# Kernel optimization log

Measured on AMD Instinct MI355X. Metric: run time of the kernel, lower is better.

Reference implementation:

```python
import jax, jax.numpy as jnp
import numpy as np

DIM = 512
NUM_HEADS = 8
B, NW, W = 8, 64, 64  # batch, num_windows, window_size


def setup_inputs() -> dict:
    key = jax.random.key(0)
    k1, k2, k3 = jax.random.split(key, 3)
    x = jax.random.normal(k1, (B, NW, W, DIM), dtype=jnp.float32)
    w_qkv = jax.random.normal(k2, (DIM, 3 * DIM), dtype=jnp.float32) * (DIM ** -0.5)
    w_proj = jax.random.normal(k3, (DIM, DIM), dtype=jnp.float32) * (DIM ** -0.5)
    b_proj = jnp.zeros((DIM,), dtype=jnp.float32)
    return {"x": x, "w_qkv": w_qkv, "w_proj": w_proj, "b_proj": b_proj}


def reference(x, w_qkv, w_proj, b_proj):
    batch, nw, w, dim = x.shape
    heads = NUM_HEADS
    dh = dim // heads
    scale = dh ** -0.5
    # qkv projection (no bias): [B, nW, W, 3*dim]
    qkv = jnp.einsum('bnwc,cd->bnwd', x, w_qkv)
    # -> [B, nW, W, 3, H, dh] -> [3, B, H, nW, W, dh]
    qkv = qkv.reshape(batch, nw, w, 3, heads, dh)
    qkv = jnp.transpose(qkv, (3, 0, 4, 1, 2, 5))
    q, k, v = qkv[0], qkv[1], qkv[2]
    # attention logits per window: [B, H, nW, W, W]
    attn = jnp.einsum('bhnqd,bhnkd->bhnqk', q, k) * scale
    attn = jax.nn.softmax(attn, axis=-1)
    # [B, H, nW, W, dh]
    out = jnp.einsum('bhnqk,bhnkd->bhnqd', attn, v)
    # faithful raw reshape (no transpose), matching the TF source
    out = out.reshape(batch, nw, w, dim)
    return jnp.einsum('bnwc,cd->bnwd', out, w_proj) + b_proj
```

## Files before the change

kernel.cpp:

```cpp
#include <hip/hip_runtime.h>
#include <hip/hip_bf16.h>

typedef __bf16 bf16_t;
typedef __bf16 bf16x4 __attribute__((ext_vector_type(4)));
typedef __bf16 bf16x8 __attribute__((ext_vector_type(8)));
typedef float f32x4 __attribute__((ext_vector_type(4)));
typedef float f32x16 __attribute__((ext_vector_type(16)));

#define GLOAD_LDS16(gp, lp) __builtin_amdgcn_global_load_lds( \
    (const __attribute__((address_space(1))) void*)(gp),      \
    (__attribute__((address_space(3))) void*)(lp), 16, 0, 0)

#define VMCNT(n) asm volatile("s_waitcnt vmcnt(" #n ")" ::: "memory")
#define SCHED_FENCE() __builtin_amdgcn_sched_barrier(0)
#define BARRIER() __builtin_amdgcn_s_barrier()

__device__ __forceinline__ int swz64(int row, int col) {
    return row * 64 + (col ^ ((row & 7) << 3));
}

__global__ __launch_bounds__(256) void transpose_cast_kernel(
    const float* __restrict__ src, bf16_t* __restrict__ dst, int R, int C)
{
    __shared__ float tile[32][33];
    const int bx = blockIdx.x;
    const int by = blockIdx.y;
    const int t  = threadIdx.x;
    const int i0 = t >> 5;
    const int j  = t & 31;
#pragma unroll
    for (int p = 0; p < 4; ++p) {
        int i = i0 + p * 8;
        tile[i][j] = src[(long)(by * 32 + i) * C + bx * 32 + j];
    }
    __syncthreads();
#pragma unroll
    for (int p = 0; p < 4; ++p) {
        int i = i0 + p * 8;
        dst[(long)(bx * 32 + i) * R + by * 32 + j] = (bf16_t)tile[j][i];
    }
}

__global__ __launch_bounds__(256) void cast_x_kernel(
    const float* __restrict__ src, bf16_t* __restrict__ dst, long n8)
{
    long i = (long)blockIdx.x * blockDim.x + threadIdx.x;
    const long stride = (long)gridDim.x * blockDim.x;
    for (; i < n8; i += stride) {
        const float* p = src + i * 8;
        f32x4 f0 = *(const f32x4*)p;
        f32x4 f1 = *(const f32x4*)(p + 4);
        bf16x8 o;
        o[0] = (bf16_t)f0[0]; o[1] = (bf16_t)f0[1];
        o[2] = (bf16_t)f0[2]; o[3] = (bf16_t)f0[3];
        o[4] = (bf16_t)f1[0]; o[5] = (bf16_t)f1[1];
        o[6] = (bf16_t)f1[2]; o[7] = (bf16_t)f1[3];
        *(bf16x8*)(dst + i * 8) = o;
    }
}

__global__ __launch_bounds__(256, 2) void qkv_attn_kernel(
    const bf16_t* __restrict__ xb,
    const bf16_t* __restrict__ wT,
    bf16_t* __restrict__ ao)
{
    __shared__ bf16_t arena[40960];
    bf16_t* const buf0 = arena;
    bf16_t* const buf1 = arena + 20480;

    const int id   = blockIdx.x;
    const int xcd  = id & 7;
    const int s    = id >> 3;
    const int pr   = xcd * 32 + (s >> 3);
    const int h    = s & 7;
    const int wid0 = pr * 2;

    const bf16_t* xw = xb + (long)wid0 * 64 * 512;

    const int t    = threadIdx.x;
    const int wv   = t >> 6;
    const int lane = t & 63;
    const int wm   = wv >> 1;
    const int wn   = wv & 1;
    const int l31  = lane & 31;
    const int l5   = lane >> 5;
    const int rlo  = lane >> 3;
    const int ch   = (lane & 7) ^ rlo;

    bf16_t* const lQw = arena +     0 + wm * 12288;
    bf16_t* const lKw = arena +  4096 + wm * 12288;
    bf16_t* const lVw = arena +  8192 + wm * 12288;
    bf16_t* const lPw = arena + 24576 + wm * 4096;

    auto stage = [&](bf16_t* buf, int k0) {
#pragma unroll
        for (int p = 0; p < 4; ++p) {
            const int rb = wv * 4 + p;
            GLOAD_LDS16(xw + (long)(rb * 8 + rlo) * 512 + k0 + ch * 8,
                        buf + rb * 512);
        }
#pragma unroll
        for (int j = 0; j < 6; ++j) {
            const int rb = wv * 6 + j;
            const int nr = rb * 8 + rlo;
            const int grow = ((nr >> 6) << 9) + h * 64 + (nr & 63);
            GLOAD_LDS16(wT + (long)grow * 512 + k0 + ch * 8,
                        buf + 8192 + rb * 512);
        }
    };

    f32x16 acc[2][3];
#pragma unroll
    for (int mi = 0; mi < 2; ++mi)
#pragma unroll
        for (int ni = 0; ni < 3; ++ni) acc[mi][ni] = (f32x16)0.0f;

    auto compute = [&](const bf16_t* lX, const bf16_t* lW) {
        __builtin_amdgcn_s_setprio(1);
#pragma unroll
        for (int ks = 0; ks < 64; ks += 16) {
            bf16x8 a0 = *(const bf16x8*)&lX[swz64(wm * 64 +  0 + l31, ks + l5 * 8)];
            bf16x8 a1 = *(const bf16x8*)&lX[swz64(wm * 64 + 32 + l31, ks + l5 * 8)];
#pragma unroll
            for (int ni = 0; ni < 3; ++ni) {
                bf16x8 b = *(const bf16x8*)&lW[swz64(wn * 96 + ni * 32 + l31, ks + l5 * 8)];
                acc[0][ni] = __builtin_amdgcn_mfma_f32_32x32x16_bf16(a0, b, acc[0][ni], 0, 0, 0);
                acc[1][ni] = __builtin_amdgcn_mfma_f32_32x32x16_bf16(a1, b, acc[1][ni], 0, 0, 0);
            }
        }
        __builtin_amdgcn_s_setprio(0);
    };

    stage(buf0, 0);
#pragma unroll 1
    for (int kc2 = 0; kc2 < 4; ++kc2) {
        const int kc = kc2 * 2;
        stage(buf1, (kc + 1) * 64);
        VMCNT(10);
        SCHED_FENCE();
        BARRIER();
        compute(buf0, buf0 + 8192);
        SCHED_FENCE();
        BARRIER();
        if (kc2 < 3) {
            stage(buf0, (kc + 2) * 64);
            VMCNT(10);
        } else {
            VMCNT(0);
        }
        SCHED_FENCE();
        BARRIER();
        compute(buf1, buf1 + 8192);
        SCHED_FENCE();
        BARRIER();
    }

#pragma unroll
    for (int mi = 0; mi < 2; ++mi) {
#pragma unroll
        for (int ni = 0; ni < 3; ++ni) {
            const int n = wn * 96 + ni * 32 + l31;
            const int g = n >> 6;
            const int c = n & 63;
            if (g == 2) {
#pragma unroll
                for (int rq = 0; rq < 4; ++rq) {
                    const int tk0 = mi * 32 + 8 * rq + 4 * l5;
                    bf16x4 pk;
                    pk[0] = (bf16_t)acc[mi][ni][rq * 4 + 0];
                    pk[1] = (bf16_t)acc[mi][ni][rq * 4 + 1];
                    pk[2] = (bf16_t)acc[mi][ni][rq * 4 + 2];
                    pk[3] = (bf16_t)acc[mi][ni][rq * 4 + 3];
                    *(bf16x4*)&lVw[swz64(c, tk0)] = pk;
                }
            } else {
#pragma unroll
                for (int r = 0; r < 16; ++r) {
                    const int tk = mi * 32 + (r & 3) + ((r >> 2) << 3) + (l5 << 2);
                    const bf16_t val = (bf16_t)acc[mi][ni][r];
                    if (g == 0) lQw[swz64(tk, c)] = val;
                    else        lKw[swz64(tk, c)] = val;
                }
            }
        }
    }
    __syncthreads();

    const int lr = lane & 15;
    const int q  = lane >> 4;
    const int qh = wn * 32;
    const float scale = 0.125f;

    f32x4 sA[2][4];
#pragma unroll
    for (int i = 0; i < 2; ++i)
#pragma unroll
        for (int j = 0; j < 4; ++j) sA[i][j] = (f32x4)0.0f;
#pragma unroll
    for (int ks = 0; ks < 64; ks += 32) {
        bf16x8 aq0 = *(const bf16x8*)&lQw[swz64(qh +  0 + lr, ks + q * 8)];
        bf16x8 aq1 = *(const bf16x8*)&lQw[swz64(qh + 16 + lr, ks + q * 8)];
#pragma unroll
        for (int j = 0; j < 4; ++j) {
            bf16x8 bk = *(const bf16x8*)&lKw[swz64(j * 16 + lr, ks + q * 8)];
            sA[0][j] = __builtin_amdgcn_mfma_f32_16x16x32_bf16(aq0, bk, sA[0][j], 0, 0, 0);
            sA[1][j] = __builtin_amdgcn_mfma_f32_16x16x32_bf16(aq1, bk, sA[1][j], 0, 0, 0);
        }
    }

#pragma unroll
    for (int i = 0; i < 2; ++i)
#pragma unroll
    for (int reg = 0; reg < 4; ++reg) {
        float m = fmaxf(fmaxf(sA[i][0][reg], sA[i][1][reg]),
                        fmaxf(sA[i][2][reg], sA[i][3][reg]));
#pragma unroll
        for (int d = 1; d < 16; d <<= 1) m = fmaxf(m, __shfl_xor(m, d));
        float p[4];
        float sum = 0.0f;
#pragma unroll
        for (int j = 0; j < 4; ++j) {
            p[j] = __expf((sA[i][j][reg] - m) * scale);
            sum += p[j];
        }
#pragma unroll
        for (int d = 1; d < 16; d <<= 1) sum += __shfl_xor(sum, d);
        const float inv = 1.0f / sum;
        const int row = qh + i * 16 + q * 4 + reg;
#pragma unroll
        for (int j = 0; j < 4; ++j)
            lPw[swz64(row, j * 16 + lr)] = (bf16_t)(p[j] * inv);
    }

    f32x4 o[2][4];
#pragma unroll
    for (int i = 0; i < 2; ++i)
#pragma unroll
        for (int d4 = 0; d4 < 4; ++d4) o[i][d4] = (f32x4)0.0f;
#pragma unroll
    for (int ks = 0; ks < 64; ks += 32) {
        bf16x8 ap0 = *(const bf16x8*)&lPw[swz64(qh +  0 + lr, ks + q * 8)];
        bf16x8 ap1 = *(const bf16x8*)&lPw[swz64(qh + 16 + lr, ks + q * 8)];
#pragma unroll
        for (int d4 = 0; d4 < 4; ++d4) {
            bf16x8 bv = *(const bf16x8*)&lVw[swz64(d4 * 16 + lr, ks + q * 8)];
            o[0][d4] = __builtin_amdgcn_mfma_f32_16x16x32_bf16(ap0, bv, o[0][d4], 0, 0, 0);
            o[1][d4] = __builtin_amdgcn_mfma_f32_16x16x32_bf16(ap1, bv, o[1][d4], 0, 0, 0);
        }
    }

    const int wid = wid0 + wm;
    const int bb  = wid >> 6;
    const int nw  = wid & 63;
    bf16_t* aop = ao + ((long)bb * 4096 + (long)h * 512 + nw * 8) * 512;
#pragma unroll
    for (int i = 0; i < 2; ++i)
#pragma unroll
    for (int d4 = 0; d4 < 4; ++d4)
#pragma unroll
    for (int reg = 0; reg < 4; ++reg) {
        const int wr = qh + i * 16 + q * 4 + reg;
        aop[(long)(wr >> 3) * 512 + (wr & 7) * 64 + d4 * 16 + lr] =
            (bf16_t)o[i][d4][reg];
    }
}

__global__ __launch_bounds__(256) void gemm2_kernel(
    const bf16_t* __restrict__ A,
    const bf16_t* __restrict__ Bt,
    const float*  __restrict__ bias,
    float* __restrict__ C,
    int M, int N, int K)
{
    __shared__ bf16_t arena[32768];
    bf16_t* const lA0 = arena;
    bf16_t* const lB0 = arena + 8192;
    bf16_t* const lA1 = arena + 16384;
    bf16_t* const lB1 = arena + 24576;

    const int tid  = threadIdx.x;
    const int wave = tid >> 6;
    const int lane = tid & 63;
    const int wm   = wave >> 1;
    const int wn   = wave & 1;
    const int lr   = lane & 15;
    const int q    = lane >> 4;
    const int rlo  = lane >> 3;
    const int ch   = (lane & 7) ^ rlo;

    const int id  = blockIdx.x;
    const int xcd = id & 7;
    const int s   = id >> 3;
    const int bm  = xcd * 32 + (s >> 2);
    const int bn  = s & 3;

    const long arow0 = (long)bm * 128;
    const long brow0 = (long)bn * 128;

    f32x4 acc[4][4];
#pragma unroll
    for (int i = 0; i < 4; ++i)
#pragma unroll
        for (int j = 0; j < 4; ++j) acc[i][j] = (f32x4)0.0f;

    auto stage = [&](bf16_t* bA, bf16_t* bB, long k0) {
#pragma unroll
        for (int p = 0; p < 4; ++p) {
            const int rb = wave * 4 + p;
            const int r  = rb * 8 + rlo;
            GLOAD_LDS16(A  + (arow0 + r) * (long)K + k0 + ch * 8, bA + rb * 512);
            GLOAD_LDS16(Bt + (brow0 + r) * (long)K + k0 + ch * 8, bB + rb * 512);
        }
    };

    auto compute = [&](const bf16_t* lA, const bf16_t* lB) {
        __builtin_amdgcn_s_setprio(1);
#pragma unroll
        for (int ks = 0; ks < 64; ks += 32) {
            bf16x8 af[4], bf[4];
#pragma unroll
            for (int i = 0; i < 4; ++i)
                af[i] = *(const bf16x8*)&lA[swz64(wm * 64 + i * 16 + lr, ks + q * 8)];
#pragma unroll
            for (int j = 0; j < 4; ++j)
                bf[j] = *(const bf16x8*)&lB[swz64(wn * 64 + j * 16 + lr, ks + q * 8)];
#pragma unroll
            for (int i = 0; i < 4; ++i)
#pragma unroll
                for (int j = 0; j < 4; ++j)
                    acc[i][j] = __builtin_amdgcn_mfma_f32_16x16x32_bf16(
                        af[i], bf[j], acc[i][j], 0, 0, 0);
        }
        __builtin_amdgcn_s_setprio(0);
    };

    stage(lA0, lB0, 0);
#pragma unroll 1
    for (int kt2 = 0; kt2 < 4; ++kt2) {
        const int kt = kt2 * 2;
        stage(lA1, lB1, (long)(kt + 1) * 64);
        VMCNT(8);
        SCHED_FENCE();
        BARRIER();
        compute(lA0, lB0);
        SCHED_FENCE();
        BARRIER();
        if (kt2 < 3) {
            stage(lA0, lB0, (long)(kt + 2) * 64);
            VMCNT(8);
        } else {
            VMCNT(0);
        }
        SCHED_FENCE();
        BARRIER();
        compute(lA1, lB1);
        SCHED_FENCE();
        BARRIER();
    }

#pragma unroll
    for (int i = 0; i < 4; ++i) {
        const long r = arow0 + wm * 64 + i * 16 + q * 4;
#pragma unroll
        for (int j = 0; j < 4; ++j) {
            const long c = brow0 + wn * 64 + j * 16 + lr;
            const float bv2 = bias[c];
#pragma unroll
            for (int reg = 0; reg < 4; ++reg) {
                C[(r + reg) * N + c] = acc[i][j][reg] + bv2;
            }
        }
    }
}

extern "C" void kernel_launch(void* const* d_in, const int* in_sizes, int n_in,
                              void* d_out, int out_size, void* d_ws, size_t ws_size,
                              hipStream_t stream)
{
    (void)in_sizes; (void)n_in; (void)out_size;
    const float* x     = (const float*)d_in[0];
    const float* wqkv  = (const float*)d_in[1];
    const float* wproj = (const float*)d_in[2];
    const float* bproj = (const float*)d_in[3];
    float* out = (float*)d_out;

    bf16_t* wT = (bf16_t*)d_ws;
    bf16_t* pT = wT + (size_t)1536 * 512;
    bf16_t* ao = pT + (size_t)512 * 512;

    const size_t base_elems = (size_t)1536 * 512 + (size_t)512 * 512
                            + (size_t)32768 * 512;
    const size_t xb_elems   = (size_t)32768 * 512;
    bf16_t* xb = (ws_size >= (base_elems + xb_elems) * sizeof(bf16_t))
               ? (ao + xb_elems)
               : (bf16_t*)d_out;

    transpose_cast_kernel<<<dim3(48, 16), 256, 0, stream>>>(wqkv, wT, 512, 1536);
    transpose_cast_kernel<<<dim3(16, 16), 256, 0, stream>>>(wproj, pT, 512, 512);
    cast_x_kernel<<<2048, 256, 0, stream>>>(x, xb, (long)32768 * 512 / 8);

    qkv_attn_kernel<<<2048, 256, 0, stream>>>(xb, wT, ao);

    gemm2_kernel<<<1024, 256, 0, stream>>>(
        ao, pT, bproj, out, 32768, 512, 512);
}
```

Before: 209.8 us.

## Load QKV GEMM X operand to registers and triple-buffer weights in LDS

In the fused QKV+attention kernel, the X tile is now loaded straight from global memory into double-buffered registers instead of being staged through LDS. Only the weight tiles go through LDS, now in a three-deep ring that needs one barrier per K-chunk instead of two. LDS use drops from 80KB to 72KB, with the P buffer aliased onto the Q region. In exchange, register pressure rises and the two wn-waves issue duplicate global loads for the same X rows.

```diff
diff --git a/kernel.cpp b/kernel.cpp
--- a/kernel.cpp
+++ b/kernel.cpp
@@ -64,9 +64,11 @@
     const bf16_t* __restrict__ wT,
     bf16_t* __restrict__ ao)
 {
-    __shared__ bf16_t arena[40960];
-    bf16_t* const buf0 = arena;
-    bf16_t* const buf1 = arena + 20480;
+    __shared__ bf16_t arena[36864];
+    bf16_t* const wb0 = arena;
+    bf16_t* const wb1 = arena + 12288;
+    bf16_t* const wb2 = arena + 24576;
+    bf16_t* const wb[3] = { wb0, wb1, wb2 };
 
     const int id   = blockIdx.x;
     const int xcd  = id & 7;
@@ -87,27 +89,29 @@
     const int rlo  = lane >> 3;
     const int ch   = (lane & 7) ^ rlo;
 
-    bf16_t* const lQw = arena +     0 + wm * 12288;
-    bf16_t* const lKw = arena +  4096 + wm * 12288;
-    bf16_t* const lVw = arena +  8192 + wm * 12288;
-    bf16_t* const lPw = arena + 24576 + wm * 4096;
-
-    auto stage = [&](bf16_t* buf, int k0) {
-#pragma unroll
-        for (int p = 0; p < 4; ++p) {
-            const int rb = wv * 4 + p;
-            GLOAD_LDS16(xw + (long)(rb * 8 + rlo) * 512 + k0 + ch * 8,
-                        buf + rb * 512);
-        }
+    bf16_t* const lQw = arena +    0 + wm * 12288;
+    bf16_t* const lKw = arena + 4096 + wm * 12288;
+    bf16_t* const lVw = arena + 8192 + wm * 12288;
+    bf16_t* const lPw = lQw;
+
+    auto stageW = [&](bf16_t* buf, int k0) {
 #pragma unroll
         for (int j = 0; j < 6; ++j) {
             const int rb = wv * 6 + j;
             const int nr = rb * 8 + rlo;
             const int grow = ((nr >> 6) << 9) + h * 64 + (nr & 63);
-            GLOAD_LDS16(wT + (long)grow * 512 + k0 + ch * 8,
-                        buf + 8192 + rb * 512);
+            GLOAD_LDS16(wT + (long)grow * 512 + k0 + ch * 8, buf + rb * 512);
         }
     };
+    auto loadx = [&](bf16x8* xr, int k0) {
+#pragma unroll
+        for (int ksi = 0; ksi < 4; ++ksi)
+#pragma unroll
+            for (int mi = 0; mi < 2; ++mi)
+                xr[ksi * 2 + mi] = *(const bf16x8*)(
+                    xw + (long)(wm * 64 + mi * 32 + l31) * 512
+                       + k0 + ksi * 16 + l5 * 8);
+    };
 
     f32x16 acc[2][3];
 #pragma unroll
@@ -115,45 +119,43 @@
 #pragma unroll
         for (int ni = 0; ni < 3; ++ni) acc[mi][ni] = (f32x16)0.0f;
 
-    auto compute = [&](const bf16_t* lX, const bf16_t* lW) {
+    auto compute = [&](const bf16x8* xr, const bf16_t* lW) {
         __builtin_amdgcn_s_setprio(1);
 #pragma unroll
-        for (int ks = 0; ks < 64; ks += 16) {
-            bf16x8 a0 = *(const bf16x8*)&lX[swz64(wm * 64 +  0 + l31, ks + l5 * 8)];
-            bf16x8 a1 = *(const bf16x8*)&lX[swz64(wm * 64 + 32 + l31, ks + l5 * 8)];
+        for (int ksi = 0; ksi < 4; ++ksi) {
+            const int ks = ksi * 16;
 #pragma unroll
             for (int ni = 0; ni < 3; ++ni) {
-                bf16x8 b = *(const bf16x8*)&lW[swz64(wn * 96 + ni * 32 + l31, ks + l5 * 8)];
-                acc[0][ni] = __builtin_amdgcn_mfma_f32_32x32x16_bf16(a0, b, acc[0][ni], 0, 0, 0);
-                acc[1][ni] = __builtin_amdgcn_mfma_f32_32x32x16_bf16(a1, b, acc[1][ni], 0, 0, 0);
+                bf16x8 b = *(const bf16x8*)&lW[swz64(wn * 96 + ni * 32 + l31,
+                                                    ks + l5 * 8)];
+                acc[0][ni] = __builtin_amdgcn_mfma_f32_32x32x16_bf16(
+                    xr[ksi * 2 + 0], b, acc[0][ni], 0, 0, 0);
+                acc[1][ni] = __builtin_amdgcn_mfma_f32_32x32x16_bf16(
+                    xr[ksi * 2 + 1], b, acc[1][ni], 0, 0, 0);
             }
         }
         __builtin_amdgcn_s_setprio(0);
     };
 
-    stage(buf0, 0);
-#pragma unroll 1
-    for (int kc2 = 0; kc2 < 4; ++kc2) {
-        const int kc = kc2 * 2;
-        stage(buf1, (kc + 1) * 64);
-        VMCNT(10);
+    bf16x8 xA[8], xB[8];
+    loadx(xA, 0);
+    stageW(wb0, 0);
+    stageW(wb1, 64);
+#pragma unroll
+    for (int tc = 0; tc < 8; ++tc) {
+        if (tc < 7) { VMCNT(6); }
+        else        { VMCNT(0); }
         SCHED_FENCE();
         BARRIER();
-        compute(buf0, buf0 + 8192);
-        SCHED_FENCE();
-        BARRIER();
-        if (kc2 < 3) {
-            stage(buf0, (kc + 2) * 64);
-            VMCNT(10);
-        } else {
-            VMCNT(0);
-        }
-        SCHED_FENCE();
-        BARRIER();
-        compute(buf1, buf1 + 8192);
-        SCHED_FENCE();
-        BARRIER();
-    }
+        SCHED_FENCE();
+        bf16x8* xcur = (tc & 1) ? xB : xA;
+        bf16x8* xnxt = (tc & 1) ? xA : xB;
+        if (tc < 7) loadx(xnxt, (tc + 1) * 64);
+        if (tc < 6) stageW(wb[(tc + 2) % 3], (tc + 2) * 64);
+        compute(xcur, wb[tc % 3]);
+    }
+    SCHED_FENCE();
+    BARRIER();
 
 #pragma unroll
     for (int mi = 0; mi < 2; ++mi) {
@@ -259,8 +261,8 @@
     for (int d4 = 0; d4 < 4; ++d4)
 #pragma unroll
     for (int reg = 0; reg < 4; ++reg) {
-        const int wr = qh + i * 16 + q * 4 + reg;
-        aop[(long)(wr >> 3) * 512 + (wr & 7) * 64 + d4 * 16 + lr] =
+        const int wr2 = qh + i * 16 + q * 4 + reg;
+        aop[(long)(wr2 >> 3) * 512 + (wr2 & 7) * 64 + d4 * 16 + lr] =
             (bf16_t)o[i][d4][reg];
     }
 }
```

Result: slower. 239.7 us (+14.3%).
